# Optimization experiments

Hardware: AMD Instinct MI355X
Metric: run time of the kernel (lower is better)

Reference implementation:

```python
import jax, jax.numpy as jnp
import numpy as np
import math

DIM = 2048
N_HEADS = 16
Q_LORA = 512
KV_LORA = 512
NOPE = 128
ROPE = 64
QK_HD = NOPE + ROPE
V_HD = 128
THETA = 1e6


def _linear_params(key, fan_in, fan_out):
    kw, kb = jax.random.split(key)
    w = jax.random.normal(kw, (fan_in, fan_out), jnp.float32) * 0.02
    b = jax.random.normal(kb, (fan_out,), jnp.float32) * 0.02
    return w, b


def setup_inputs() -> dict:
    key = jax.random.key(0)
    ks = jax.random.split(key, 6)
    x = jax.random.normal(ks[0], (2, 2048, DIM), jnp.float32)
    wq_a_w, wq_a_b = _linear_params(ks[1], DIM, Q_LORA)
    wq_b_w, wq_b_b = _linear_params(ks[2], Q_LORA, N_HEADS * QK_HD)
    wkv_a_w, wkv_a_b = _linear_params(ks[3], DIM, KV_LORA + ROPE)
    wkv_b_w, wkv_b_b = _linear_params(ks[4], KV_LORA, N_HEADS * (NOPE + V_HD))
    wo_w, wo_b = _linear_params(ks[5], N_HEADS * V_HD, DIM)
    return {"x": x,
            "wq_a_w": wq_a_w, "wq_a_b": wq_a_b,
            "wq_b_w": wq_b_w, "wq_b_b": wq_b_b,
            "wkv_a_w": wkv_a_w, "wkv_a_b": wkv_a_b,
            "wkv_b_w": wkv_b_w, "wkv_b_b": wkv_b_b,
            "wo_w": wo_w, "wo_b": wo_b}


def _rope_cos_sin(seq_len):
    # freqs = 1/theta^(2i/ROPE), i in [0, ROPE/2)
    inv_freq = 1.0 / (THETA ** (jnp.arange(0, ROPE, 2, dtype=jnp.float32) / ROPE))
    t = jnp.arange(seq_len, dtype=jnp.float32)
    freqs = jnp.outer(t, inv_freq)  # (S, ROPE/2)
    return jnp.cos(freqs), jnp.sin(freqs)


def _apply_rope(x, cos, sin):
    # x: (B, S, H, ROPE); pairs (even, odd) form complex numbers
    xr = x[..., 0::2]
    xi = x[..., 1::2]
    c = cos[None, :, None, :]
    s = sin[None, :, None, :]
    out_r = xr * c - xi * s
    out_i = xr * s + xi * c
    return jnp.stack([out_r, out_i], axis=-1).reshape(x.shape)


def reference(x, wq_a_w, wq_a_b, wq_b_w, wq_b_b, wkv_a_w, wkv_a_b,
              wkv_b_w, wkv_b_b, wo_w, wo_b):
    bs, seq_len, _ = x.shape
    # low-rank Q projection
    q = (x @ wq_a_w + wq_a_b) @ wq_b_w + wq_b_b
    q = q.reshape(bs, seq_len, N_HEADS, QK_HD)
    q_nope, q_pe = q[..., :NOPE], q[..., NOPE:]
    # compressed KV + decoupled rope key
    ckv = x @ wkv_a_w + wkv_a_b
    compressed_kv, k_pe = ckv[..., :KV_LORA], ckv[..., KV_LORA:]
    k_pe = k_pe.reshape(bs, seq_len, 1, ROPE)
    kv = (compressed_kv @ wkv_b_w + wkv_b_b).reshape(bs, seq_len, N_HEADS, NOPE + V_HD)
    kv_nope, v = kv[..., :NOPE], kv[..., NOPE:]
    # partial RoPE
    cos, sin = _rope_cos_sin(seq_len)
    q_pe = _apply_rope(q_pe, cos, sin)
    k_pe = _apply_rope(k_pe, cos, sin)
    k_pe = jnp.broadcast_to(k_pe, (bs, seq_len, N_HEADS, ROPE))
    qf = jnp.concatenate([q_nope, q_pe], axis=-1)   # (B,S,H,QK_HD)
    kf = jnp.concatenate([kv_nope, k_pe], axis=-1)  # (B,S,H,QK_HD)
    # full attention (no mask, scale by sqrt(v_head_dim) per source)
    scores = jnp.einsum('bqhd,bkhd->bhqk', qf, kf) / math.sqrt(V_HD)
    probs = jax.nn.softmax(scores.astype(jnp.float32), axis=-1).astype(qf.dtype)
    out = jnp.einsum('bhqk,bkhd->bqhd', probs, v)
    out = out.reshape(bs, seq_len, N_HEADS * V_HD)
    return out @ wo_w + wo_b
```

## Files before the change

### kernel.cpp

```cpp
#include <hip/hip_runtime.h>
#include <hip/hip_bf16.h>


typedef __attribute__((ext_vector_type(8))) short short8;
typedef __attribute__((ext_vector_type(4))) short short4v;
typedef __attribute__((ext_vector_type(4))) float f32x4;

#define GLOAD_LDS16(gp, lp)                                                      \
  __builtin_amdgcn_global_load_lds((const __attribute__((address_space(1))) void*)(gp), \
                                   (__attribute__((address_space(3))) void*)(lp), 16, 0, 0)

static __device__ __forceinline__ unsigned short bf16_bits(float f) {
  __hip_bfloat16 h = __float2bfloat16(f);
  return __builtin_bit_cast(unsigned short, h);
}
static __device__ __forceinline__ float bf16_to_f(unsigned short u) {
  unsigned int v = (unsigned int)u << 16;
  return __builtin_bit_cast(float, v);
}


__global__ void k_f32_to_bf16(const float* __restrict__ in, unsigned short* __restrict__ out, int n4) {
  int i = blockIdx.x * 256 + threadIdx.x;
  if (i >= n4) return;
  float4 v = reinterpret_cast<const float4*>(in)[i];
  ushort4 o;
  o.x = bf16_bits(v.x); o.y = bf16_bits(v.y); o.z = bf16_bits(v.z); o.w = bf16_bits(v.w);
  reinterpret_cast<ushort4*>(out)[i] = o;
}

__global__ void k_transpose_bf16(const float* __restrict__ W, unsigned short* __restrict__ Wt,
                                 int K, int N) {
  __shared__ float tile[32][33];
  int k0 = blockIdx.x * 32, n0 = blockIdx.y * 32;
  int tx = threadIdx.x & 31, ty = threadIdx.x >> 5;
#pragma unroll
  for (int i = 0; i < 32; i += 8) {
    int k = k0 + ty + i, n = n0 + tx;
    tile[ty + i][tx] = (k < K && n < N) ? W[(size_t)k * N + n] : 0.f;
  }
  __syncthreads();
#pragma unroll
  for (int i = 0; i < 32; i += 8) {
    int n = n0 + ty + i, k = k0 + tx;
    if (n < N && k < K) Wt[(size_t)n * K + k] = bf16_bits(tile[tx][ty + i]);
  }
}


__global__ void k_rope_table(float2* __restrict__ cs) {
  int idx = blockIdx.x * 256 + threadIdx.x;
  int s = idx >> 5, i = idx & 31;
  float inv = powf(1.0e6f, -(float)(2 * i) / 64.0f);
  float a = (float)s * inv;
  cs[idx] = make_float2(cosf(a), sinf(a));
}

__global__ void k_rope_q(unsigned short* __restrict__ q, const float2* __restrict__ cs) {
  int idx = blockIdx.x * 256 + threadIdx.x;
  int i = idx & 31;
  int h = (idx >> 5) & 15;
  int bs = idx >> 9;
  int s = bs & 2047;
  size_t base = (size_t)bs * 3072 + h * 192 + 128 + 2 * i;
  float xr = bf16_to_f(q[base]);
  float xi = bf16_to_f(q[base + 1]);
  float2 c = cs[(s << 5) + i];
  q[base]     = bf16_bits(xr * c.x - xi * c.y);
  q[base + 1] = bf16_bits(xr * c.y + xi * c.x);
}

__global__ void k_rope_k(unsigned short* __restrict__ ckv, const float2* __restrict__ cs) {
  int idx = blockIdx.x * 256 + threadIdx.x;
  int i = idx & 31;
  int bs = idx >> 5;
  int s = bs & 2047;
  size_t base = (size_t)bs * 576 + 512 + 2 * i;
  float xr = bf16_to_f(ckv[base]);
  float xi = bf16_to_f(ckv[base + 1]);
  float2 c = cs[(s << 5) + i];
  ckv[base]     = bf16_bits(xr * c.x - xi * c.y);
  ckv[base + 1] = bf16_bits(xr * c.y + xi * c.x);
}


template <typename OutT>
__global__ __launch_bounds__(256, 2) void k_gemm(const unsigned short* __restrict__ A, int lda,
                                                 const unsigned short* __restrict__ Wt,
                                                 const float* __restrict__ bias,
                                                 OutT* __restrict__ C, int M, int N, int K) {
  __shared__ unsigned short lA[128][64];
  __shared__ unsigned short lB[128][64];
  int m0 = blockIdx.x * 128, n0 = blockIdx.y * 128;
  int t = threadIdx.x;
  int lane = t & 63, wid = t >> 6;
  int g = lane >> 4, col = lane & 15;
  int wr = wid >> 1, wc = wid & 1;
  int srow = lane >> 3;
  int schunk = (lane & 7) ^ srow;
  f32x4 acc[4][4] = {};

  for (int kt = 0; kt < K; kt += 64) {
#pragma unroll
    for (int i = 0; i < 4; ++i) {
      int rowb = 32 * wid + 8 * i;
      int row = rowb + srow;
      GLOAD_LDS16(&A[(size_t)(m0 + row) * lda + kt + 8 * schunk], &lA[rowb][0]);
      GLOAD_LDS16(&Wt[(size_t)(n0 + row) * K + kt + 8 * schunk], &lB[rowb][0]);
    }
    __syncthreads();
#pragma unroll
    for (int kk = 0; kk < 64; kk += 32) {
      int ch = (kk >> 3) + g;
      int sl = 8 * (ch ^ (col & 7));
      short8 a[4], b[4];
#pragma unroll
      for (int mf = 0; mf < 4; ++mf)
        a[mf] = *reinterpret_cast<const short8*>(&lA[64 * wr + 16 * mf + col][sl]);
#pragma unroll
      for (int nf = 0; nf < 4; ++nf)
        b[nf] = *reinterpret_cast<const short8*>(&lB[64 * wc + 16 * nf + col][sl]);
#pragma unroll
      for (int mf = 0; mf < 4; ++mf)
#pragma unroll
        for (int nf = 0; nf < 4; ++nf)
          acc[mf][nf] = __builtin_amdgcn_mfma_f32_16x16x32_bf16(a[mf], b[nf], acc[mf][nf], 0, 0, 0);
    }
    __syncthreads();
  }

#pragma unroll
  for (int mf = 0; mf < 4; ++mf) {
#pragma unroll
    for (int nf = 0; nf < 4; ++nf) {
      int n = n0 + 64 * wc + 16 * nf + col;
      if (n >= N) continue;
      float bv = bias[n];
#pragma unroll
      for (int r = 0; r < 4; ++r) {
        int m = m0 + 64 * wr + 16 * mf + 4 * g + r;
        float v = acc[mf][nf][r] + bv;
        if constexpr (sizeof(OutT) == 4)
          C[(size_t)m * N + n] = v;
        else
          C[(size_t)m * N + n] = bf16_bits(v);
      }
    }
  }
}


__global__ __launch_bounds__(512, 2) void k_attn(const unsigned short* __restrict__ q,
                                                 const unsigned short* __restrict__ ckv,
                                                 const unsigned short* __restrict__ kv,
                                                 unsigned short* __restrict__ out) {
  __shared__ unsigned short lK[64][200];
  __shared__ unsigned short lV[128][72];
  __shared__ unsigned short lP[8][16][72];
  int bx = blockIdx.x;
  int qt = bx & 15, h = (bx >> 4) & 15, b = bx >> 8;
  int t = threadIdx.x, lane = t & 63, w = t >> 6;
  int g = lane >> 4, col = lane & 15;
  int q0 = qt * 128;
  int bb = b * 2048;
  const float scale = 0.08838834764831845f;

  short8 qf[6];
  {
    int srow = bb + q0 + 16 * w + col;
    size_t base = ((size_t)srow * 16 + h) * 192 + 8 * g;
#pragma unroll
    for (int j = 0; j < 6; ++j)
      qf[j] = *reinterpret_cast<const short8*>(&q[base + 32 * j]);
  }

  short8 kreg[3];
  short4v vreg0[2], vreg1[2];

  auto load_tile = [&](int k0) {
#pragma unroll
    for (int it = 0; it < 3; ++it) {
      int c = t + 512 * it;
      int row = c / 24, cc = c % 24;
      int s = bb + k0 + row;
      const unsigned short* src;
      if (cc < 16) src = &kv[((size_t)s * 16 + h) * 256 + cc * 8];
      else         src = &ckv[(size_t)s * 576 + 512 + (cc - 16) * 8];
      kreg[it] = *reinterpret_cast<const short8*>(src);
    }
#pragma unroll
    for (int it = 0; it < 2; ++it) {
      int c = t + 512 * it;
      int kp = c >> 5, dv0 = (c & 31) * 4;
      size_t vb = ((size_t)(bb + k0 + 2 * kp) * 16 + h) * 256 + 128 + dv0;
      vreg0[it] = *reinterpret_cast<const short4v*>(&kv[vb]);
      vreg1[it] = *reinterpret_cast<const short4v*>(&kv[vb + 4096]);
    }
  };

  load_tile(0);

  f32x4 o[8] = {};
  float mrow[4] = {-1e30f, -1e30f, -1e30f, -1e30f};
  float lrow[4] = {0.f, 0.f, 0.f, 0.f};

  for (int k0 = 0; k0 < 2048; k0 += 64) {
    __syncthreads();
#pragma unroll
    for (int it = 0; it < 3; ++it) {
      int c = t + 512 * it;
      int row = c / 24, cc = c % 24;
      *reinterpret_cast<short8*>(&lK[row][cc * 8]) = kreg[it];
    }
#pragma unroll
    for (int it = 0; it < 2; ++it) {
      int c = t + 512 * it;
      int kp = c >> 5, dv0 = (c & 31) * 4;
      int k2 = 2 * kp;
#pragma unroll
      for (int j = 0; j < 4; ++j) {
        int dv = dv0 + j;
        int phys = (((k2 >> 3) ^ ((dv >> 3) & 7)) << 3) + (k2 & 7);
        unsigned int pw = (unsigned int)(unsigned short)vreg0[it][j] |
                          ((unsigned int)(unsigned short)vreg1[it][j] << 16);
        *reinterpret_cast<unsigned int*>(&lV[dv][phys]) = pw;
      }
    }
    __syncthreads();
    if (k0 + 64 < 2048) load_tile(k0 + 64);
    __builtin_amdgcn_sched_barrier(0);

    f32x4 sf[4];
    __builtin_amdgcn_s_setprio(1);
#pragma unroll
    for (int c = 0; c < 4; ++c) {
      f32x4 acc = {};
#pragma unroll
      for (int j = 0; j < 6; ++j) {
        short8 bfr = *reinterpret_cast<const short8*>(&lK[16 * c + col][32 * j + 8 * g]);
        acc = __builtin_amdgcn_mfma_f32_16x16x32_bf16(qf[j], bfr, acc, 0, 0, 0);
      }
      sf[c] = acc;
    }
    __builtin_amdgcn_s_setprio(0);

#pragma unroll
    for (int r = 0; r < 4; ++r) {
      float tm = -1e30f;
#pragma unroll
      for (int c = 0; c < 4; ++c) { sf[c][r] *= scale; tm = fmaxf(tm, sf[c][r]); }
#pragma unroll
      for (int off = 8; off; off >>= 1) tm = fmaxf(tm, __shfl_xor(tm, off, 64));
      float mn = fmaxf(mrow[r], tm);
      float rs = __expf(mrow[r] - mn);
      mrow[r] = mn;
      float ps = 0.f;
#pragma unroll
      for (int c = 0; c < 4; ++c) { float p = __expf(sf[c][r] - mn); sf[c][r] = p; ps += p; }
#pragma unroll
      for (int off = 8; off; off >>= 1) ps += __shfl_xor(ps, off, 64);
      lrow[r] = lrow[r] * rs + ps;
#pragma unroll
      for (int n = 0; n < 8; ++n) o[n][r] *= rs;
    }

#pragma unroll
    for (int c = 0; c < 4; ++c)
#pragma unroll
      for (int r = 0; r < 4; ++r)
        lP[w][4 * g + r][16 * c + col] = bf16_bits(sf[c][r]);
    __builtin_amdgcn_s_setprio(1);
#pragma unroll
    for (int kk = 0; kk < 64; kk += 32) {
      short8 pa = *reinterpret_cast<const short8*>(&lP[w][col][kk + 8 * g]);
#pragma unroll
      for (int n = 0; n < 8; ++n) {
        int dv = 16 * n + col;
        int phys = ((((kk + 8 * g) >> 3) ^ ((dv >> 3) & 7)) << 3);
        short8 bv = *reinterpret_cast<const short8*>(&lV[dv][phys]);
        o[n] = __builtin_amdgcn_mfma_f32_16x16x32_bf16(pa, bv, o[n], 0, 0, 0);
      }
    }
    __builtin_amdgcn_s_setprio(0);
  }

#pragma unroll
  for (int r = 0; r < 4; ++r) {
    float inv = 1.0f / lrow[r];
    int srow = bb + q0 + 16 * w + 4 * g + r;
    size_t base = (size_t)srow * 2048 + h * 128;
#pragma unroll
    for (int n = 0; n < 8; ++n)
      out[base + 16 * n + col] = bf16_bits(o[n][r] * inv);
  }
}


extern "C" void kernel_launch(void* const* d_in, const int* in_sizes, int n_in,
                              void* d_out, int out_size, void* d_ws, size_t ws_size,
                              hipStream_t stream) {
  const float* x       = (const float*)d_in[0];
  const float* wq_a_w  = (const float*)d_in[1];
  const float* wq_a_b  = (const float*)d_in[2];
  const float* wq_b_w  = (const float*)d_in[3];
  const float* wq_b_b  = (const float*)d_in[4];
  const float* wkv_a_w = (const float*)d_in[5];
  const float* wkv_a_b = (const float*)d_in[6];
  const float* wkv_b_w = (const float*)d_in[7];
  const float* wkv_b_b = (const float*)d_in[8];
  const float* wo_w    = (const float*)d_in[9];
  const float* wo_b    = (const float*)d_in[10];
  float* out = (float*)d_out;

  const int BS = 4096;
  char* p = (char*)d_ws;
  auto alloc = [&](size_t bytes) { char* r = p; p += (bytes + 255) & ~(size_t)255; return r; };
  unsigned short* xb    = (unsigned short*)alloc((size_t)BS * 2048 * 2);
  unsigned short* wqat  = (unsigned short*)alloc((size_t)512 * 2048 * 2);
  unsigned short* wqbt  = (unsigned short*)alloc((size_t)3072 * 512 * 2);
  unsigned short* wkvat = (unsigned short*)alloc((size_t)640 * 2048 * 2);
  unsigned short* wkvbt = (unsigned short*)alloc((size_t)4096 * 512 * 2);
  unsigned short* wot   = (unsigned short*)alloc((size_t)2048 * 2048 * 2);
  unsigned short* qa    = (unsigned short*)alloc((size_t)BS * 512 * 2);
  unsigned short* qbuf  = (unsigned short*)alloc((size_t)BS * 3072 * 2);
  unsigned short* ckv   = (unsigned short*)alloc((size_t)BS * 576 * 2);
  unsigned short* kvbuf = (unsigned short*)alloc((size_t)BS * 4096 * 2);
  unsigned short* attno = (unsigned short*)alloc((size_t)BS * 2048 * 2);
  float2* cs            = (float2*)alloc((size_t)2048 * 32 * sizeof(float2));

  k_f32_to_bf16<<<BS * 2048 / 4 / 256, 256, 0, stream>>>(x, xb, BS * 2048 / 4);
  k_transpose_bf16<<<dim3(2048 / 32, 512 / 32), 256, 0, stream>>>(wq_a_w, wqat, 2048, 512);
  k_transpose_bf16<<<dim3(512 / 32, 3072 / 32), 256, 0, stream>>>(wq_b_w, wqbt, 512, 3072);
  k_transpose_bf16<<<dim3(2048 / 32, 576 / 32), 256, 0, stream>>>(wkv_a_w, wkvat, 2048, 576);
  k_transpose_bf16<<<dim3(512 / 32, 4096 / 32), 256, 0, stream>>>(wkv_b_w, wkvbt, 512, 4096);
  k_transpose_bf16<<<dim3(2048 / 32, 2048 / 32), 256, 0, stream>>>(wo_w, wot, 2048, 2048);
  k_rope_table<<<2048 * 32 / 256, 256, 0, stream>>>(cs);

  k_gemm<unsigned short><<<dim3(BS / 128, 512 / 128), 256, 0, stream>>>(
      xb, 2048, wqat, wq_a_b, qa, BS, 512, 2048);
  k_gemm<unsigned short><<<dim3(BS / 128, 3072 / 128), 256, 0, stream>>>(
      qa, 512, wqbt, wq_b_b, qbuf, BS, 3072, 512);
  k_gemm<unsigned short><<<dim3(BS / 128, (576 + 127) / 128), 256, 0, stream>>>(
      xb, 2048, wkvat, wkv_a_b, ckv, BS, 576, 2048);
  k_rope_q<<<BS * 16 * 32 / 256, 256, 0, stream>>>(qbuf, cs);
  k_rope_k<<<BS * 32 / 256, 256, 0, stream>>>(ckv, cs);
  k_gemm<unsigned short><<<dim3(BS / 128, 4096 / 128), 256, 0, stream>>>(
      ckv, 576, wkvbt, wkv_b_b, kvbuf, BS, 4096, 512);
  k_attn<<<2 * 16 * 16, 512, 0, stream>>>(qbuf, ckv, kvbuf, attno);
  k_gemm<float><<<dim3(BS / 128, 2048 / 128), 256, 0, stream>>>(
      attno, 2048, wot, wo_b, out, BS, 2048, 2048);
}
```

Before: 501.9 us.

## Process two 16-row query tiles per wave in attention kernel

Each wave now handles 32 query rows instead of 16, so a block covers 256 queries and the grid is halved. Every K and V fragment read from LDS feeds two MFMAs, which halves LDS traffic and the global K/V tile loads per query. The cost is higher register pressure from doubled accumulators and Q fragments, with launch_bounds(512,2) possibly forcing spills, and fewer blocks (256) on a GPU with many CUs, which may cut occupancy.

```diff
diff --git a/kernel.cpp b/kernel.cpp
--- a/kernel.cpp
+++ b/kernel.cpp
@@ -156,22 +156,23 @@
                                                  unsigned short* __restrict__ out) {
   __shared__ unsigned short lK[64][200];
   __shared__ unsigned short lV[128][72];
-  __shared__ unsigned short lP[8][16][72];
+  __shared__ unsigned short lP[8][32][72];
   int bx = blockIdx.x;
-  int qt = bx & 15, h = (bx >> 4) & 15, b = bx >> 8;
+  int qt = bx & 7, h = (bx >> 3) & 15, b = bx >> 7;
   int t = threadIdx.x, lane = t & 63, w = t >> 6;
   int g = lane >> 4, col = lane & 15;
-  int q0 = qt * 128;
+  int q0 = qt * 256;
   int bb = b * 2048;
   const float scale = 0.08838834764831845f;
 
-  short8 qf[6];
-  {
-    int srow = bb + q0 + 16 * w + col;
+  short8 qf[2][6];
+#pragma unroll
+  for (int m = 0; m < 2; ++m) {
+    int srow = bb + q0 + 32 * w + 16 * m + col;
     size_t base = ((size_t)srow * 16 + h) * 192 + 8 * g;
 #pragma unroll
     for (int j = 0; j < 6; ++j)
-      qf[j] = *reinterpret_cast<const short8*>(&q[base + 32 * j]);
+      qf[m][j] = *reinterpret_cast<const short8*>(&q[base + 32 * j]);
   }
 
   short8 kreg[3];
@@ -200,9 +201,9 @@
 
   load_tile(0);
 
-  f32x4 o[8] = {};
-  float mrow[4] = {-1e30f, -1e30f, -1e30f, -1e30f};
-  float lrow[4] = {0.f, 0.f, 0.f, 0.f};
+  f32x4 o[2][8] = {};
+  float mrow[2][4] = {{-1e30f, -1e30f, -1e30f, -1e30f}, {-1e30f, -1e30f, -1e30f, -1e30f}};
+  float lrow[2][4] = {};
 
   for (int k0 = 0; k0 < 2048; k0 += 64) {
     __syncthreads();
@@ -230,68 +231,81 @@
     if (k0 + 64 < 2048) load_tile(k0 + 64);
     __builtin_amdgcn_sched_barrier(0);
 
-    f32x4 sf[4];
+    f32x4 sf[2][4] = {};
     __builtin_amdgcn_s_setprio(1);
 #pragma unroll
     for (int c = 0; c < 4; ++c) {
-      f32x4 acc = {};
 #pragma unroll
       for (int j = 0; j < 6; ++j) {
         short8 bfr = *reinterpret_cast<const short8*>(&lK[16 * c + col][32 * j + 8 * g]);
-        acc = __builtin_amdgcn_mfma_f32_16x16x32_bf16(qf[j], bfr, acc, 0, 0, 0);
-      }
-      sf[c] = acc;
+#pragma unroll
+        for (int m = 0; m < 2; ++m)
+          sf[m][c] = __builtin_amdgcn_mfma_f32_16x16x32_bf16(qf[m][j], bfr, sf[m][c], 0, 0, 0);
+      }
     }
     __builtin_amdgcn_s_setprio(0);
 
 #pragma unroll
-    for (int r = 0; r < 4; ++r) {
-      float tm = -1e30f;
-#pragma unroll
-      for (int c = 0; c < 4; ++c) { sf[c][r] *= scale; tm = fmaxf(tm, sf[c][r]); }
-#pragma unroll
-      for (int off = 8; off; off >>= 1) tm = fmaxf(tm, __shfl_xor(tm, off, 64));
-      float mn = fmaxf(mrow[r], tm);
-      float rs = __expf(mrow[r] - mn);
-      mrow[r] = mn;
-      float ps = 0.f;
-#pragma unroll
-      for (int c = 0; c < 4; ++c) { float p = __expf(sf[c][r] - mn); sf[c][r] = p; ps += p; }
-#pragma unroll
-      for (int off = 8; off; off >>= 1) ps += __shfl_xor(ps, off, 64);
-      lrow[r] = lrow[r] * rs + ps;
-#pragma unroll
-      for (int n = 0; n < 8; ++n) o[n][r] *= rs;
-    }
-
-#pragma unroll
-    for (int c = 0; c < 4; ++c)
-#pragma unroll
-      for (int r = 0; r < 4; ++r)
-        lP[w][4 * g + r][16 * c + col] = bf16_bits(sf[c][r]);
+    for (int m = 0; m < 2; ++m) {
+#pragma unroll
+      for (int r = 0; r < 4; ++r) {
+        float tm = -1e30f;
+#pragma unroll
+        for (int c = 0; c < 4; ++c) { sf[m][c][r] *= scale; tm = fmaxf(tm, sf[m][c][r]); }
+#pragma unroll
+        for (int off = 8; off; off >>= 1) tm = fmaxf(tm, __shfl_xor(tm, off, 64));
+        float mn = fmaxf(mrow[m][r], tm);
+        float rs = __expf(mrow[m][r] - mn);
+        mrow[m][r] = mn;
+        float ps = 0.f;
+#pragma unroll
+        for (int c = 0; c < 4; ++c) { float p = __expf(sf[m][c][r] - mn); sf[m][c][r] = p; ps += p; }
+#pragma unroll
+        for (int off = 8; off; off >>= 1) ps += __shfl_xor(ps, off, 64);
+        lrow[m][r] = lrow[m][r] * rs + ps;
+#pragma unroll
+        for (int n = 0; n < 8; ++n) o[m][n][r] *= rs;
+      }
+    }
+
+#pragma unroll
+    for (int m = 0; m < 2; ++m)
+#pragma unroll
+      for (int c = 0; c < 4; ++c)
+#pragma unroll
+        for (int r = 0; r < 4; ++r)
+          lP[w][16 * m + 4 * g + r][16 * c + col] = bf16_bits(sf[m][c][r]);
     __builtin_amdgcn_s_setprio(1);
 #pragma unroll
     for (int kk = 0; kk < 64; kk += 32) {
-      short8 pa = *reinterpret_cast<const short8*>(&lP[w][col][kk + 8 * g]);
+      short8 pa[2];
+#pragma unroll
+      for (int m = 0; m < 2; ++m)
+        pa[m] = *reinterpret_cast<const short8*>(&lP[w][16 * m + col][kk + 8 * g]);
 #pragma unroll
       for (int n = 0; n < 8; ++n) {
         int dv = 16 * n + col;
         int phys = ((((kk + 8 * g) >> 3) ^ ((dv >> 3) & 7)) << 3);
         short8 bv = *reinterpret_cast<const short8*>(&lV[dv][phys]);
-        o[n] = __builtin_amdgcn_mfma_f32_16x16x32_bf16(pa, bv, o[n], 0, 0, 0);
+#pragma unroll
+        for (int m = 0; m < 2; ++m)
+          o[m][n] = __builtin_amdgcn_mfma_f32_16x16x32_bf16(pa[m], bv, o[m][n], 0, 0, 0);
       }
     }
     __builtin_amdgcn_s_setprio(0);
   }
 
 #pragma unroll
-  for (int r = 0; r < 4; ++r) {
-    float inv = 1.0f / lrow[r];
-    int srow = bb + q0 + 16 * w + 4 * g + r;
-    size_t base = (size_t)srow * 2048 + h * 128;
-#pragma unroll
-    for (int n = 0; n < 8; ++n)
-      out[base + 16 * n + col] = bf16_bits(o[n][r] * inv);
+  for (int m = 0; m < 2; ++m) {
+#pragma unroll
+    for (int r = 0; r < 4; ++r) {
+      float inv = 1.0f / lrow[m][r];
+      int srow = bb + q0 + 32 * w + 16 * m + 4 * g + r;
+      size_t base = (size_t)srow * 2048 + h * 128;
+#pragma unroll
+      for (int n = 0; n < 8; ++n)
+        out[base + 16 * n + col] = bf16_bits(o[m][n][r] * inv);
+    }
   }
 }
 
@@ -346,7 +360,7 @@
   k_rope_k<<<BS * 32 / 256, 256, 0, stream>>>(ckv, cs);
   k_gemm<unsigned short><<<dim3(BS / 128, 4096 / 128), 256, 0, stream>>>(
       ckv, 576, wkvbt, wkv_b_b, kvbuf, BS, 4096, 512);
-  k_attn<<<2 * 16 * 16, 512, 0, stream>>>(qbuf, ckv, kvbuf, attno);
+  k_attn<<<2 * 16 * 8, 512, 0, stream>>>(qbuf, ckv, kvbuf, attno);
   k_gemm<float><<<dim3(BS / 128, 2048 / 128), 256, 0, stream>>>(
       attno, 2048, wot, wo_b, out, BS, 2048, 2048);
 }
```

Measured after the change: 477.3 us. 4.9% less time.
